# Kernel optimization log

Measured on AMD Instinct MI355X. Metric: run time of the kernel, lower is better.

## Reference

```python
import jax, jax.numpy as jnp
import numpy as np

L, H, D, HS, DFF, V, B, T = 4, 16, 1024, 64, 5120, 32000, 2, 1024
EPS = 1e-5


def setup_inputs() -> dict:
    key = jax.random.key(0)
    ks = iter(jax.random.split(key, 40))
    def nrm(shape):
        return jax.random.normal(next(ks), shape, dtype=jnp.float32) * 0.02
    inp = {}
    inp['idx'] = jax.random.randint(next(ks), (B, T), 0, V)
    inp['tok_emb'] = nrm((V, D))
    inp['pos_emb'] = nrm((T, D))
    for s in ('u', 'm'):  # u = unmasked heads, m = masked (causal) heads
        inp['Wq_' + s] = nrm((L, H, D, HS)); inp['bq_' + s] = jnp.zeros((L, H, HS), jnp.float32)
        inp['Wk_' + s] = nrm((L, H, D, HS)); inp['bk_' + s] = jnp.zeros((L, H, HS), jnp.float32)
        inp['Wv_' + s] = nrm((L, H, D, HS)); inp['bv_' + s] = jnp.zeros((L, H, HS), jnp.float32)
        inp['Wp_' + s] = nrm((L, D, D));     inp['bp_' + s] = jnp.zeros((L, D), jnp.float32)
    inp['W1'] = nrm((L, D, DFF)); inp['b1'] = jnp.zeros((L, DFF), jnp.float32)
    inp['W2'] = nrm((L, DFF, D)); inp['b2'] = jnp.zeros((L, D), jnp.float32)
    ones = jnp.ones((L, D), jnp.float32); zer = jnp.zeros((L, D), jnp.float32)
    inp['lnf_g'] = ones; inp['lnf_b'] = zer     # LayerNorm inside FeedForward
    inp['n1_g'] = ones;  inp['n1_b'] = zer      # Block.norm1
    inp['n2_g'] = ones;  inp['n2_b'] = zer      # Block.norm2
    inp['nf_g'] = jnp.ones((D,), jnp.float32); inp['nf_b'] = jnp.zeros((D,), jnp.float32)
    inp['Wfin'] = nrm((D, V)); inp['bfin'] = jnp.zeros((V,), jnp.float32)
    return inp


def _ln(x, g, b):
    mu = jnp.mean(x, -1, keepdims=True)
    var = jnp.mean((x - mu) ** 2, -1, keepdims=True)
    return (x - mu) / jnp.sqrt(var + EPS) * g + b


def _attn(xn, Wq, bq, Wk, bk, Wv, bv, Wp, bp, causal):
    # xn: [B,T,D]; Wq/Wk/Wv: [H,D,HS] (all heads batched in one einsum)
    q = jnp.einsum('btd,hde->bhte', xn, Wq) + bq[:, None, :]
    k = jnp.einsum('btd,hde->bhte', xn, Wk) + bk[:, None, :]
    v = jnp.einsum('btd,hde->bhte', xn, Wv) + bv[:, None, :]
    w = jnp.einsum('bhte,bhse->bhts', q, k) * (HS ** -0.5)
    if causal:
        mask = jnp.tril(jnp.ones((w.shape[-2], w.shape[-1]), bool))
        w = jnp.where(mask, w, -jnp.inf)
    w = jax.nn.softmax(w, axis=-1)
    o = jnp.einsum('bhts,bhse->bhte', w, v)
    o = o.transpose(0, 2, 1, 3).reshape(xn.shape[0], xn.shape[1], -1)  # concat heads
    return o @ Wp + bp


def _ffn(x, W1, b1, W2, b2, g, b):
    h = jax.nn.leaky_relu(x @ W1 + b1, negative_slope=0.01)
    return _ln(h @ W2 + b2, g, b)


def reference(idx, tok_emb, pos_emb,
              Wq_u, bq_u, Wk_u, bk_u, Wv_u, bv_u, Wp_u, bp_u,
              Wq_m, bq_m, Wk_m, bk_m, Wv_m, bv_m, Wp_m, bp_m,
              W1, b1, W2, b2, lnf_g, lnf_b, n1_g, n1_b, n2_g, n2_b,
              nf_g, nf_b, Wfin, bfin):
    Tn = idx.shape[1]
    x = tok_emb[idx] + pos_emb[:Tn]
    for l in range(L):
        # exact quirky Block wiring from the original code
        x2 = x + _attn(_ln(x, n1_g[l], n1_b[l]), Wq_u[l], bq_u[l], Wk_u[l], bk_u[l],
                       Wv_u[l], bv_u[l], Wp_u[l], bp_u[l], False)
        x = x2 + _ln(_ffn(_ln(x2, n2_g[l], n2_b[l]), W1[l], b1[l], W2[l], b2[l],
                          lnf_g[l], lnf_b[l]), n1_g[l], n1_b[l])
        x2 = x + _attn(_ln(x, n1_g[l], n1_b[l]), Wq_m[l], bq_m[l], Wk_m[l], bk_m[l],
                       Wv_m[l], bv_m[l], Wp_m[l], bp_m[l], True)
        x = x2 + _ln(_ffn(_ln(x2, n2_g[l], n2_b[l]), W1[l], b1[l], W2[l], b2[l],
                          lnf_g[l], lnf_b[l]), n2_g[l], n2_b[l])
    x = _ln(x, nf_g, nf_b)
    return x @ Wfin + bfin  # logits [B,T,V]; targets=None path -> loss is None
```

## Files before the change

kernel.cpp:

```cpp
#include <hip/hip_runtime.h>
#include <hip/hip_bf16.h>
#include <math.h>

#define LNUM 4
#define H 16
#define D 1024
#define HS 64
#define DFF 5120
#define V 32000
#define BB 2
#define T 1024
#define M (BB*T)
#define EPS 1e-5f

typedef __attribute__((ext_vector_type(8))) short bf16x8;
typedef __attribute__((ext_vector_type(4))) float f32x4;

__device__ __forceinline__ void gload16(const void* g, void* l) {
    __builtin_amdgcn_global_load_lds(
        (const __attribute__((address_space(1))) void*)g,
        (__attribute__((address_space(3))) void*)l, 16, 0, 0);
}

__device__ __forceinline__ float wred_sum(float v) {
    #pragma unroll
    for (int off = 32; off; off >>= 1) v += __shfl_xor(v, off, 64);
    return v;
}

__global__ __launch_bounds__(256) void embed_kernel(const int* __restrict__ idx,
        const float* __restrict__ tok, const float* __restrict__ pos,
        float* __restrict__ x) {
    int row = blockIdx.x;
    int t = row & (T - 1);
    int tok_id = idx[row];
    int c = threadIdx.x * 4;
    float4 a = *(const float4*)&tok[(size_t)tok_id * D + c];
    float4 p = *(const float4*)&pos[(size_t)t * D + c];
    a.x += p.x; a.y += p.y; a.z += p.z; a.w += p.w;
    *(float4*)&x[(size_t)row * D + c] = a;
}

__global__ __launch_bounds__(256) void ln_bf16_w4_kernel(const float* __restrict__ in,
        const float* __restrict__ g, const float* __restrict__ b,
        __hip_bfloat16* __restrict__ out) {
    int w = threadIdx.x >> 6, lane = threadIdx.x & 63;
    int row = blockIdx.x * 4 + w;
    const float* rp = in + (size_t)row * D;
    float4 xv[4];
    float s = 0.f;
    #pragma unroll
    for (int c = 0; c < 4; ++c) {
        xv[c] = *(const float4*)&rp[c * 256 + lane * 4];
        s += xv[c].x + xv[c].y + xv[c].z + xv[c].w;
    }
    float mu = wred_sum(s) * (1.0f / D);
    float vs = 0.f;
    #pragma unroll
    for (int c = 0; c < 4; ++c) {
        xv[c].x -= mu; xv[c].y -= mu; xv[c].z -= mu; xv[c].w -= mu;
        vs += xv[c].x*xv[c].x + xv[c].y*xv[c].y + xv[c].z*xv[c].z + xv[c].w*xv[c].w;
    }
    float rs = rsqrtf(wred_sum(vs) * (1.0f / D) + EPS);
    #pragma unroll
    for (int c = 0; c < 4; ++c) {
        int j = c * 256 + lane * 4;
        float4 gv = *(const float4*)&g[j];
        float4 bv = *(const float4*)&b[j];
        union { ushort4 u4; __hip_bfloat16 h[4]; } pk;
        pk.h[0] = __float2bfloat16(xv[c].x * rs * gv.x + bv.x);
        pk.h[1] = __float2bfloat16(xv[c].y * rs * gv.y + bv.y);
        pk.h[2] = __float2bfloat16(xv[c].z * rs * gv.z + bv.z);
        pk.h[3] = __float2bfloat16(xv[c].w * rs * gv.w + bv.w);
        *(ushort4*)&out[(size_t)row * D + j] = pk.u4;
    }
}

template<int NP>
__global__ __launch_bounds__(256) void ffn_tail_kernel(
        const float* __restrict__ part, const float* __restrict__ b2,
        const float* __restrict__ g1, const float* __restrict__ b1,
        const float* __restrict__ g2, const float* __restrict__ b2g,
        const float* __restrict__ res, float* __restrict__ xout,
        const float* __restrict__ gn, const float* __restrict__ bn,
        __hip_bfloat16* __restrict__ xnout) {
    const size_t MD = (size_t)M * D;
    int w = threadIdx.x >> 6, lane = threadIdx.x & 63;
    int row = blockIdx.x * 4 + w;
    size_t ro = (size_t)row * D;
    float4 f[4];
    float s = 0.f;
    #pragma unroll
    for (int c = 0; c < 4; ++c) {
        int j = c * 256 + lane * 4;
        float4 acc = *(const float4*)&b2[j];
        #pragma unroll
        for (int pI = 0; pI < NP; ++pI) {
            float4 pv = *(const float4*)&part[pI * MD + ro + j];
            acc.x += pv.x; acc.y += pv.y; acc.z += pv.z; acc.w += pv.w;
        }
        f[c] = acc;
        s += acc.x + acc.y + acc.z + acc.w;
    }
    float mu = wred_sum(s) * (1.0f / D);
    float vs = 0.f;
    #pragma unroll
    for (int c = 0; c < 4; ++c) {
        f[c].x -= mu; f[c].y -= mu; f[c].z -= mu; f[c].w -= mu;
        vs += f[c].x*f[c].x + f[c].y*f[c].y + f[c].z*f[c].z + f[c].w*f[c].w;
    }
    float rs = rsqrtf(wred_sum(vs) * (1.0f / D) + EPS);
    float s2 = 0.f;
    #pragma unroll
    for (int c = 0; c < 4; ++c) {
        int j = c * 256 + lane * 4;
        float4 gv = *(const float4*)&g1[j];
        float4 bv = *(const float4*)&b1[j];
        f[c].x = f[c].x * rs * gv.x + bv.x;
        f[c].y = f[c].y * rs * gv.y + bv.y;
        f[c].z = f[c].z * rs * gv.z + bv.z;
        f[c].w = f[c].w * rs * gv.w + bv.w;
        s2 += f[c].x + f[c].y + f[c].z + f[c].w;
    }
    float mu2 = wred_sum(s2) * (1.0f / D);
    float vs2 = 0.f;
    #pragma unroll
    for (int c = 0; c < 4; ++c) {
        f[c].x -= mu2; f[c].y -= mu2; f[c].z -= mu2; f[c].w -= mu2;
        vs2 += f[c].x*f[c].x + f[c].y*f[c].y + f[c].z*f[c].z + f[c].w*f[c].w;
    }
    float rs2 = rsqrtf(wred_sum(vs2) * (1.0f / D) + EPS);
    float s3 = 0.f;
    #pragma unroll
    for (int c = 0; c < 4; ++c) {
        int j = c * 256 + lane * 4;
        float4 gv = *(const float4*)&g2[j];
        float4 bv = *(const float4*)&b2g[j];
        float4 rv = *(const float4*)&res[ro + j];
        f[c].x = rv.x + f[c].x * rs2 * gv.x + bv.x;
        f[c].y = rv.y + f[c].y * rs2 * gv.y + bv.y;
        f[c].z = rv.z + f[c].z * rs2 * gv.z + bv.z;
        f[c].w = rv.w + f[c].w * rs2 * gv.w + bv.w;
        *(float4*)&xout[ro + j] = f[c];
        s3 += f[c].x + f[c].y + f[c].z + f[c].w;
    }
    float mu3 = wred_sum(s3) * (1.0f / D);
    float vs3 = 0.f;
    #pragma unroll
    for (int c = 0; c < 4; ++c) {
        f[c].x -= mu3; f[c].y -= mu3; f[c].z -= mu3; f[c].w -= mu3;
        vs3 += f[c].x*f[c].x + f[c].y*f[c].y + f[c].z*f[c].z + f[c].w*f[c].w;
    }
    float rs3 = rsqrtf(wred_sum(vs3) * (1.0f / D) + EPS);
    #pragma unroll
    for (int c = 0; c < 4; ++c) {
        int j = c * 256 + lane * 4;
        float4 gv = *(const float4*)&gn[j];
        float4 bv = *(const float4*)&bn[j];
        union { ushort4 u4; __hip_bfloat16 h[4]; } pk;
        pk.h[0] = __float2bfloat16(f[c].x * rs3 * gv.x + bv.x);
        pk.h[1] = __float2bfloat16(f[c].y * rs3 * gv.y + bv.y);
        pk.h[2] = __float2bfloat16(f[c].z * rs3 * gv.z + bv.z);
        pk.h[3] = __float2bfloat16(f[c].w * rs3 * gv.w + bv.w);
        *(ushort4*)&xnout[ro + j] = pk.u4;
    }
}

__global__ __launch_bounds__(256) void transpose_bf16_kernel(
        const float* __restrict__ in, __hip_bfloat16* __restrict__ out,
        int R, int C, size_t zin, size_t zout) {
    __shared__ float t[32][33];
    in += (size_t)blockIdx.z * zin; out += (size_t)blockIdx.z * zout;
    int tx = threadIdx.x & 31, ty = threadIdx.x >> 5;
    int c0 = blockIdx.x * 32, r0 = blockIdx.y * 32;
    #pragma unroll
    for (int i = 0; i < 4; ++i)
        t[ty + i * 8][tx] = in[(size_t)(r0 + ty + i * 8) * C + c0 + tx];
    __syncthreads();
    #pragma unroll
    for (int i = 0; i < 4; ++i)
        out[(size_t)(c0 + ty + i * 8) * R + r0 + tx] = __float2bfloat16(t[tx][ty + i * 8]);
}

__global__ __launch_bounds__(256) void transpose_qkv_kernel(
        const float* __restrict__ Wq, const float* __restrict__ Wk,
        const float* __restrict__ Wv, short* __restrict__ outT) {
    __shared__ float t[32][33];
    int z = blockIdx.z;
    int which = z >> 4, h = z & 15;
    const float* in = (which == 0 ? Wq : which == 1 ? Wk : Wv) + (size_t)h * D * HS;
    __hip_bfloat16* out = (__hip_bfloat16*)outT + ((size_t)which * H + h) * HS * D;
    int tx = threadIdx.x & 31, ty = threadIdx.x >> 5;
    int c0 = blockIdx.x * 32, r0 = blockIdx.y * 32;
    #pragma unroll
    for (int i = 0; i < 4; ++i)
        t[ty + i * 8][tx] = in[(size_t)(r0 + ty + i * 8) * HS + c0 + tx];
    __syncthreads();
    #pragma unroll
    for (int i = 0; i < 4; ++i)
        out[(size_t)(c0 + ty + i * 8) * D + r0 + tx] = __float2bfloat16(t[tx][ty + i * 8]);
}

__global__ __launch_bounds__(256) void transpose_v_kernel(const short* __restrict__ in,
        short* __restrict__ out) {
    __shared__ short t[32][33];
    int z = blockIdx.z;
    in  += (size_t)z * T * HS;
    out += (size_t)z * HS * T;
    int tx = threadIdx.x & 31, ty = threadIdx.x >> 5;
    int c0 = blockIdx.x * 32, r0 = blockIdx.y * 32;
    #pragma unroll
    for (int i = 0; i < 4; ++i)
        t[ty + i * 8][tx] = in[(size_t)(r0 + ty + i * 8) * HS + c0 + tx];
    __syncthreads();
    #pragma unroll
    for (int i = 0; i < 4; ++i)
        out[(size_t)(c0 + ty + i * 8) * T + r0 + tx] = t[tx][ty + i * 8];
}

template<int BM, int EPI>
__global__ __launch_bounds__(256) void mm_bf16_kernel(
        const short* __restrict__ A, const short* __restrict__ BT,
        const float* __restrict__ bias0, const float* __restrict__ bias1,
        const float* __restrict__ bias2, const float* __restrict__ res,
        float* __restrict__ C0, float* __restrict__ C1, float* __restrict__ C2,
        __hip_bfloat16* __restrict__ Cbf, int N, int Kloop, int lda) {
    constexpr int BK = 64, BN = 128;
    constexpr int MI = BM / 32;
    __shared__ __align__(16) char As[2][BM * 128];
    __shared__ __align__(16) char Bs[2][BN * 128];
    int nwg = gridDim.x * gridDim.y;
    int bid = blockIdx.y * gridDim.x + blockIdx.x;
    int bx = blockIdx.x, by = blockIdx.y;
    if (!(nwg & 7)) {
        int s = (bid & 7) * (nwg >> 3) + (bid >> 3);
        bx = s % gridDim.x; by = s / gridDim.x;
    }
    int tid = threadIdx.x;
    int lane = tid & 63, wid = tid >> 6;
    int wr = wid >> 1, wc = wid & 1;
    int l15 = lane & 15, l16 = lane >> 4;
    int m0 = bx * BM, n0 = by * BN;
    f32x4 acc[MI][4] = {};

    const size_t lda2 = (size_t)lda * 2;
    const char* Agc = (const char*)A + (size_t)m0 * lda2 + (size_t)blockIdx.z * Kloop * 2;
    const char* Bgc = (const char*)BT + (size_t)n0 * lda2 + (size_t)blockIdx.z * Kloop * 2;

    auto stage = [&](int buf, int kbyte) {
        #pragma unroll
        for (int i = 0; i < BM / 32; ++i) {
            int o = i * 4096 + tid * 16;
            int row = o >> 7, col = o & 127;
            gload16(Agc + (size_t)row * lda2 + kbyte + (col ^ ((row & 7) << 4)),
                    As[buf] + o);
        }
        #pragma unroll
        for (int i = 0; i < 4; ++i) {
            int o = i * 4096 + tid * 16;
            int row = o >> 7, col = o & 127;
            gload16(Bgc + (size_t)row * lda2 + kbyte + (col ^ ((row & 7) << 4)),
                    Bs[buf] + o);
        }
    };
    auto compute = [&](int buf) {
        #pragma unroll
        for (int kk = 0; kk < 2; ++kk) {
            bf16x8 af[MI], bfr[4];
            #pragma unroll
            for (int mi = 0; mi < MI; ++mi) {
                int row = wr * (BM / 2) + mi * 16 + l15;
                af[mi] = *(const bf16x8*)(As[buf] + row * 128 +
                          ((kk * 64 + l16 * 16) ^ ((row & 7) << 4)));
            }
            #pragma unroll
            for (int ni = 0; ni < 4; ++ni) {
                int row = wc * 64 + ni * 16 + l15;
                bfr[ni] = *(const bf16x8*)(Bs[buf] + row * 128 +
                          ((kk * 64 + l16 * 16) ^ ((row & 7) << 4)));
            }
            __builtin_amdgcn_s_setprio(1);
            #pragma unroll
            for (int mi = 0; mi < MI; ++mi)
                #pragma unroll
                for (int ni = 0; ni < 4; ++ni)
                    acc[mi][ni] = __builtin_amdgcn_mfma_f32_16x16x32_bf16(
                        af[mi], bfr[ni], acc[mi][ni], 0, 0, 0);
            __builtin_amdgcn_s_setprio(0);
        }
    };

    const int NT = Kloop / BK;
    stage(0, 0);
    stage(1, 128);
    for (int t = 0; t < NT; ++t) {
        if (t < NT - 1) {
            if constexpr (BM == 128) asm volatile("s_waitcnt vmcnt(8)" ::: "memory");
            else                     asm volatile("s_waitcnt vmcnt(6)" ::: "memory");
        } else {
            asm volatile("s_waitcnt vmcnt(0)" ::: "memory");
        }
        __builtin_amdgcn_sched_barrier(0);
        __builtin_amdgcn_s_barrier();
        __builtin_amdgcn_sched_barrier(0);
        compute(t & 1);
        __builtin_amdgcn_s_barrier();
        __builtin_amdgcn_sched_barrier(0);
        if (t + 2 < NT) stage(t & 1, (t + 2) * 128);
    }

    int rbase = m0 + wr * (BM / 2) + l16 * 4;
    int cbase = n0 + wc * 64 + l15;
    size_t zoff = (EPI == 4) ? (size_t)blockIdx.z * M * N : 0;
    #pragma unroll
    for (int mi = 0; mi < MI; ++mi) {
        #pragma unroll
        for (int ni = 0; ni < 4; ++ni) {
            int col = cbase + ni * 16;
            float bv = 0.f;
            if (EPI == 3) {
                int z = col >> 10, nn = col & 1023;
                bv = (z == 0 ? bias0 : z == 1 ? bias1 : bias2)[nn];
            } else if (EPI != 4) bv = bias0[col];
            #pragma unroll
            for (int r = 0; r < 4; ++r) {
                int row = rbase + mi * 16 + r;
                float v = acc[mi][ni][r] + bv;
                if (EPI == 0) {
                    C0[(size_t)row * N + col] = v;
                } else if (EPI == 1) {
                    C0[(size_t)row * N + col] = v + res[(size_t)row * N + col];
                } else if (EPI == 2) {
                    v = v > 0.f ? v : 0.01f * v;
                    Cbf[(size_t)row * N + col] = __float2bfloat16(v);
                } else if (EPI == 4) {
                    C0[zoff + (size_t)row * N + col] = v;
                } else {
                    int z = col >> 10;
                    int hh = (col >> 6) & 15, e = col & 63;
                    int b = row >> 10, t = row & (T - 1);
                    __hip_bfloat16* dst = (__hip_bfloat16*)(z == 0 ? C0 : (z == 1 ? C1 : C2));
                    dst[(((size_t)(b * H + hh)) * T + t) * HS + e] = __float2bfloat16(v);
                }
            }
        }
    }
}

template<int CAUSAL>
__global__ __launch_bounds__(256) void attn_mfma_kernel(
        const short* __restrict__ q, const short* __restrict__ k,
        const short* __restrict__ vt, __hip_bfloat16* __restrict__ att) {
    __shared__ __align__(16) short Ks[128 * 64];
    __shared__ __align__(16) short Vs[64 * 128];
    __shared__ __align__(16) short Ps[4][16 * 128];
    int bh = blockIdx.y;
    int bI = bh >> 4, h = bh & 15;
    int tix = blockIdx.x;
    if (CAUSAL) tix = (tix & 1) ? (15 - (tix >> 1)) : (tix >> 1);
    int t0 = tix * 64;
    int tid = threadIdx.x;
    int lane = tid & 63, w = tid >> 6;
    int l15 = lane & 15, l16 = lane >> 4;

    const short* Qg = q + ((size_t)bh * T + t0 + w * 16 + l15) * HS + l16 * 8;
    bf16x8 qf0 = *(const bf16x8*)Qg;
    bf16x8 qf1 = *(const bf16x8*)(Qg + 32);

    const char* Kg = (const char*)(k + (size_t)bh * T * HS);
    const char* Vg = (const char*)(vt + (size_t)bh * HS * T);

    float m_run[4] = {-1e30f, -1e30f, -1e30f, -1e30f};
    float l_run[4] = {0.f, 0.f, 0.f, 0.f};
    f32x4 acc_o[4] = {};
    char* Pw = (char*)Ps[w];
    int pswz = l15 << 4;

    int n_tiles = CAUSAL ? (t0 / 128 + 1) : (T / 128);
    for (int it = 0; it < n_tiles; ++it) {
        int s0 = it * 128;
        __syncthreads();
        #pragma unroll
        for (int i = 0; i < 4; ++i) {
            int o = i * 4096 + tid * 16;
            int row = o >> 7, bir = o & 127;
            gload16(Kg + (size_t)(s0 + row) * 128 + (bir ^ ((row & 7) << 4)),
                    (char*)Ks + o);
        }
        #pragma unroll
        for (int i = 0; i < 4; ++i) {
            int o = i * 4096 + tid * 16;
            int row = o >> 8, bb = o & 255;
            gload16(Vg + (size_t)row * 2048 + s0 * 2 + (bb ^ ((row & 15) << 4)),
                    (char*)Vs + o);
        }
        __syncthreads();

        f32x4 acc_s[8] = {};
        __builtin_amdgcn_s_setprio(1);
        #pragma unroll
        for (int c = 0; c < 8; ++c) {
            int row = c * 16 + l15;
            const char* kb_ = (const char*)Ks + row * 128;
            int swz = (row & 7) << 4;
            bf16x8 kf0 = *(const bf16x8*)(kb_ + ((l16 * 16) ^ swz));
            bf16x8 kf1 = *(const bf16x8*)(kb_ + ((64 + l16 * 16) ^ swz));
            acc_s[c] = __builtin_amdgcn_mfma_f32_16x16x32_bf16(qf0, kf0, acc_s[c], 0, 0, 0);
            acc_s[c] = __builtin_amdgcn_mfma_f32_16x16x32_bf16(qf1, kf1, acc_s[c], 0, 0, 0);
        }
        __builtin_amdgcn_s_setprio(0);

        bool domask = CAUSAL && (it == n_tiles - 1);
        #pragma unroll
        for (int r = 0; r < 4; ++r) {
            float sc[8];
            #pragma unroll
            for (int c = 0; c < 8; ++c) {
                float s = acc_s[c][r];
                if (domask && (s0 + c * 16 + l15) > (t0 + w * 16 + l16 * 4 + r)) s = -1e30f;
                sc[c] = s;
            }
            float tm = fmaxf(fmaxf(fmaxf(sc[0], sc[1]), fmaxf(sc[2], sc[3])),
                             fmaxf(fmaxf(sc[4], sc[5]), fmaxf(sc[6], sc[7])));
            tm = fmaxf(tm, __shfl_xor(tm, 1, 16));
            tm = fmaxf(tm, __shfl_xor(tm, 2, 16));
            tm = fmaxf(tm, __shfl_xor(tm, 4, 16));
            tm = fmaxf(tm, __shfl_xor(tm, 8, 16));
            float mn = fmaxf(m_run[r], tm);
            int prow = l16 * 4 + r;
            int pswzr = prow << 4;
            float ls = 0.f;
            #pragma unroll
            for (int c = 0; c < 8; ++c) {
                float pv = __expf(0.125f * (sc[c] - mn));
                int pbyte = prow * 256 + (((c * 16 + l15) * 2) ^ pswzr);
                *(__hip_bfloat16*)(Pw + pbyte) = __float2bfloat16(pv);
                ls += pv;
            }
            ls += __shfl_xor(ls, 1, 16);
            ls += __shfl_xor(ls, 2, 16);
            ls += __shfl_xor(ls, 4, 16);
            ls += __shfl_xor(ls, 8, 16);
            float alpha = __expf(0.125f * (m_run[r] - mn));
            l_run[r] = l_run[r] * alpha + ls;
            m_run[r] = mn;
            acc_o[0][r] *= alpha; acc_o[1][r] *= alpha;
            acc_o[2][r] *= alpha; acc_o[3][r] *= alpha;
        }

        const char* Pb = Pw + l15 * 256;
        bf16x8 pa[4];
        #pragma unroll
        for (int t = 0; t < 4; ++t)
            pa[t] = *(const bf16x8*)(Pb + ((t * 64 + l16 * 16) ^ pswz));
        __builtin_amdgcn_s_setprio(1);
        #pragma unroll
        for (int ni = 0; ni < 4; ++ni) {
            int row = ni * 16 + l15;
            const char* vb_ = (const char*)Vs + row * 256;
            int swz = (row & 15) << 4;
            #pragma unroll
            for (int t = 0; t < 4; ++t) {
                bf16x8 vf = *(const bf16x8*)(vb_ + ((t * 64 + l16 * 16) ^ swz));
                acc_o[ni] = __builtin_amdgcn_mfma_f32_16x16x32_bf16(pa[t], vf, acc_o[ni], 0, 0, 0);
            }
        }
        __builtin_amdgcn_s_setprio(0);
    }

    float inv[4];
    #pragma unroll
    for (int r = 0; r < 4; ++r) inv[r] = 1.0f / l_run[r];
    #pragma unroll
    for (int ni = 0; ni < 4; ++ni) {
        #pragma unroll
        for (int r = 0; r < 4; ++r) {
            size_t orow = ((size_t)(bI * T) + t0 + w * 16 + l16 * 4 + r) * D
                        + h * HS + ni * 16 + l15;
            att[orow] = __float2bfloat16(acc_o[ni][r] * inv[r]);
        }
    }
}

extern "C" void kernel_launch(void* const* d_in, const int* in_sizes, int n_in,
                              void* d_out, int out_size, void* d_ws, size_t ws_size,
                              hipStream_t stream) {
    const int*   idx     = (const int*)d_in[0];
    const float* tok_emb = (const float*)d_in[1];
    const float* pos_emb = (const float*)d_in[2];
    const float* Wq_u = (const float*)d_in[3],  *bq_u = (const float*)d_in[4];
    const float* Wk_u = (const float*)d_in[5],  *bk_u = (const float*)d_in[6];
    const float* Wv_u = (const float*)d_in[7],  *bv_u = (const float*)d_in[8];
    const float* Wp_u = (const float*)d_in[9],  *bp_u = (const float*)d_in[10];
    const float* Wq_m = (const float*)d_in[11], *bq_m = (const float*)d_in[12];
    const float* Wk_m = (const float*)d_in[13], *bk_m = (const float*)d_in[14];
    const float* Wv_m = (const float*)d_in[15], *bv_m = (const float*)d_in[16];
    const float* Wp_m = (const float*)d_in[17], *bp_m = (const float*)d_in[18];
    const float* W1   = (const float*)d_in[19], *b1   = (const float*)d_in[20];
    const float* W2   = (const float*)d_in[21], *b2   = (const float*)d_in[22];
    const float* lnf_g = (const float*)d_in[23], *lnf_b = (const float*)d_in[24];
    const float* n1_g  = (const float*)d_in[25], *n1_b  = (const float*)d_in[26];
    const float* n2_g  = (const float*)d_in[27], *n2_b  = (const float*)d_in[28];
    const float* nf_g  = (const float*)d_in[29], *nf_b  = (const float*)d_in[30];
    const float* Wfin  = (const float*)d_in[31], *bfin  = (const float*)d_in[32];
    float* out = (float*)d_out;

    char* p = (char*)d_ws;
    auto alloc = [&](size_t bytes) { char* r = p; p += (bytes + 255) & ~255ull; return r; };
    float* x    = (float*)alloc((size_t)M * D * 4);
    float* x2   = (float*)alloc((size_t)M * D * 4);
    float* w2p  = (float*)alloc((size_t)4 * M * D * 4);
    short* qbf  = (short*)alloc((size_t)M * D * 2);
    short* kbf  = (short*)alloc((size_t)M * D * 2);
    short* vbf  = (short*)alloc((size_t)M * D * 2);
    short* vtb  = (short*)alloc((size_t)M * D * 2);
    short* xnb  = (short*)alloc((size_t)M * D * 2);
    short* attb = (short*)alloc((size_t)M * D * 2);
    short* hb   = (short*)alloc((size_t)M * DFF * 2);
    short* WqkvT= (short*)alloc((size_t)3 * 1024 * 1024 * 2);
    short* WpT  = (short*)alloc((size_t)1024 * 1024 * 2);
    short* W1T  = (short*)alloc((size_t)D * DFF * 2);
    short* W2T  = (short*)alloc((size_t)DFF * D * 2);
    short* WfT  = (short*)alloc((size_t)D * V * 2);

    embed_kernel<<<M, 256, 0, stream>>>(idx, tok_emb, pos_emb, x);
    ln_bf16_w4_kernel<<<M / 4, 256, 0, stream>>>(x, n1_g, n1_b, (__hip_bfloat16*)xnb);
    transpose_bf16_kernel<<<dim3(V / 32, D / 32, 1), 256, 0, stream>>>(
        Wfin, (__hip_bfloat16*)WfT, D, V, 0, 0);

    for (int l = 0; l < LNUM; ++l) {
        const float *n1g = n1_g + l * D, *n1b = n1_b + l * D;
        const float *n2g = n2_g + l * D, *n2b = n2_b + l * D;
        const float *lfg = lnf_g + l * D, *lfb = lnf_b + l * D;
        const float *W1l = W1 + (size_t)l * D * DFF, *b1l = b1 + l * DFF;
        const float *W2l = W2 + (size_t)l * DFF * D, *b2l = b2 + l * D;
        transpose_bf16_kernel<<<dim3(DFF / 32, D / 32, 1), 256, 0, stream>>>(
            W1l, (__hip_bfloat16*)W1T, D, DFF, 0, 0);
        transpose_bf16_kernel<<<dim3(D / 32, DFF / 32, 1), 256, 0, stream>>>(
            W2l, (__hip_bfloat16*)W2T, DFF, D, 0, 0);
        for (int half = 0; half < 2; ++half) {
            const float *Wq_, *bq_, *Wk_, *bk_, *Wv_, *bv_, *Wp_, *bp_;
            if (half == 0) { Wq_ = Wq_u; bq_ = bq_u; Wk_ = Wk_u; bk_ = bk_u;
                             Wv_ = Wv_u; bv_ = bv_u; Wp_ = Wp_u; bp_ = bp_u; }
            else           { Wq_ = Wq_m; bq_ = bq_m; Wk_ = Wk_m; bk_ = bk_m;
                             Wv_ = Wv_m; bv_ = bv_m; Wp_ = Wp_m; bp_ = bp_m; }
            Wq_ += (size_t)l * H * D * HS;  bq_ += l * H * HS;
            Wk_ += (size_t)l * H * D * HS;  bk_ += l * H * HS;
            Wv_ += (size_t)l * H * D * HS;  bv_ += l * H * HS;
            Wp_ += (size_t)l * D * D;       bp_ += l * D;

            transpose_qkv_kernel<<<dim3(HS / 32, D / 32, 48), 256, 0, stream>>>(
                Wq_, Wk_, Wv_, WqkvT);
            transpose_bf16_kernel<<<dim3(D / 32, D / 32, 1), 256, 0, stream>>>(
                Wp_, (__hip_bfloat16*)WpT, D, D, 0, 0);

            mm_bf16_kernel<128, 3><<<dim3(M / 128, 3072 / 128), 256, 0, stream>>>(
                xnb, WqkvT, bq_, bk_, bv_, nullptr,
                (float*)qbf, (float*)kbf, (float*)vbf, nullptr, 3072, D, D);
            transpose_v_kernel<<<dim3(HS / 32, T / 32, BB * H), 256, 0, stream>>>(vbf, vtb);
            if (half == 0)
                attn_mfma_kernel<0><<<dim3(T / 64, BB * H), 256, 0, stream>>>(
                    qbf, kbf, vtb, (__hip_bfloat16*)attb);
            else
                attn_mfma_kernel<1><<<dim3(T / 64, BB * H), 256, 0, stream>>>(
                    qbf, kbf, vtb, (__hip_bfloat16*)attb);
            mm_bf16_kernel<64, 1><<<dim3(M / 64, D / 128), 256, 0, stream>>>(
                attb, WpT, bp_, nullptr, nullptr, x, x2, nullptr, nullptr, nullptr, D, D, D);
            ln_bf16_w4_kernel<<<M / 4, 256, 0, stream>>>(x2, n2g, n2b, (__hip_bfloat16*)xnb);
            mm_bf16_kernel<128, 2><<<dim3(M / 128, DFF / 128), 256, 0, stream>>>(
                xnb, W1T, b1l, nullptr, nullptr, nullptr, nullptr, nullptr, nullptr,
                (__hip_bfloat16*)hb, DFF, D, D);
            mm_bf16_kernel<128, 4><<<dim3(M / 128, D / 128, 4), 256, 0, stream>>>(
                hb, W2T, nullptr, nullptr, nullptr, nullptr, w2p, nullptr, nullptr,
                nullptr, D, DFF / 4, DFF);
            const float* og = half ? n2g : n1g;
            const float* ob = half ? n2b : n1b;
            const float* gn; const float* bn;
            if (half == 0)      { gn = n1g; bn = n1b; }
            else if (l < LNUM-1){ gn = n1_g + (l+1)*D; bn = n1_b + (l+1)*D; }
            else                { gn = nf_g; bn = nf_b; }
            ffn_tail_kernel<4><<<M / 4, 256, 0, stream>>>(
                w2p, b2l, lfg, lfb, og, ob, x2, x, gn, bn, (__hip_bfloat16*)xnb);
        }
    }
    mm_bf16_kernel<128, 0><<<dim3(M / 128, V / 128), 256, 0, stream>>>(
        xnb, WfT, bfin, nullptr, nullptr, nullptr, out, nullptr, nullptr, nullptr, V, D, D);
}
```

Measured before the change: 1.650 ms.

## Add 256x256-tile 512-thread GEMM kernel for FFN up-projection and logits

Adds a new GEMM kernel with 256x256 output tiles, 8 waves per block, K split into two 32-wide halves with interleaved LDS staging and MFMA phases, and XCD-aware block remapping. It replaces the 128x128 kernel for the W1 up-projection (with leaky-ReLU bf16 epilogue) and the final vocabulary projection. Larger tiles raise arithmetic intensity and cut redundant global/L2 traffic for these large GEMMs. The cost is heavier register pressure, fewer blocks (160 for W1, 1000 for logits), and a mapping that hardcodes M/256 = 8 row tiles.

```diff
diff --git a/kernel.cpp b/kernel.cpp
--- a/kernel.cpp
+++ b/kernel.cpp
@@ -218,6 +218,138 @@
         out[(size_t)(c0 + ty + i * 8) * T + r0 + tx] = t[tx][ty + i * 8];
 }
 
+template<int EPI>
+__global__ __launch_bounds__(512, 2) void mm256_kernel(
+        const short* __restrict__ A, const short* __restrict__ BT,
+        const float* __restrict__ bias0, float* __restrict__ C0,
+        __hip_bfloat16* __restrict__ Cbf, int N, int Kloop, int lda) {
+    __shared__ __align__(16) char LA[2][2][256 * 64];
+    __shared__ __align__(16) char LB[2][2][256 * 64];
+    int tid = threadIdx.x;
+    int lane = tid & 63, wid = tid >> 6;
+    int wr = wid >> 2, wc = wid & 3;
+    int l15 = lane & 15, l16 = lane >> 4;
+
+    int nwg = gridDim.x;
+    int bid = blockIdx.x;
+    int q = nwg >> 3, r = nwg & 7;
+    int xcd = bid & 7, loc = bid >> 3;
+    int wg = (xcd < r ? xcd * (q + 1) : r * (q + 1) + (xcd - r) * q) + loc;
+    int m0 = (wg & 7) * 256;
+    int n0 = (wg >> 3) * 256;
+
+    const size_t lda2 = (size_t)lda * 2;
+    const char* Agc = (const char*)A + (size_t)m0 * lda2;
+    const char* Bgc = (const char*)BT + (size_t)n0 * lda2;
+
+    f32x4 acc[8][4] = {};
+    bf16x8 af[8], bfr[2];
+
+    auto stA = [&](int buf, int kh, int kt) {
+        #pragma unroll
+        for (int i = 0; i < 2; ++i) {
+            int o = i * 8192 + tid * 16;
+            int row = o >> 6, col = o & 63;
+            gload16(Agc + (size_t)row * lda2 + kt * 128 + kh * 64 +
+                    (col ^ (((row >> 1) & 3) << 4)), LA[buf][kh] + o);
+        }
+    };
+    auto stB = [&](int buf, int kh, int kt) {
+        #pragma unroll
+        for (int i = 0; i < 2; ++i) {
+            int o = i * 8192 + tid * 16;
+            int row = o >> 6, col = o & 63;
+            gload16(Bgc + (size_t)row * lda2 + kt * 128 + kh * 64 +
+                    (col ^ (((row >> 1) & 3) << 4)), LB[buf][kh] + o);
+        }
+    };
+    auto rdA = [&](int buf, int kk) {
+        #pragma unroll
+        for (int mf = 0; mf < 8; ++mf) {
+            int row = wr * 128 + mf * 16 + l15;
+            af[mf] = *(const bf16x8*)(LA[buf][kk] + row * 64 +
+                      ((l16 * 16) ^ (((row >> 1) & 3) << 4)));
+        }
+    };
+    auto rdB = [&](int buf, int kk, int nh) {
+        #pragma unroll
+        for (int nf = 0; nf < 2; ++nf) {
+            int row = wc * 64 + nh * 32 + nf * 16 + l15;
+            bfr[nf] = *(const bf16x8*)(LB[buf][kk] + row * 64 +
+                       ((l16 * 16) ^ (((row >> 1) & 3) << 4)));
+        }
+    };
+    auto mfma16 = [&](int nh) {
+        __builtin_amdgcn_s_setprio(1);
+        #pragma unroll
+        for (int mf = 0; mf < 8; ++mf) {
+            acc[mf][nh * 2 + 0] = __builtin_amdgcn_mfma_f32_16x16x32_bf16(
+                af[mf], bfr[0], acc[mf][nh * 2 + 0], 0, 0, 0);
+            acc[mf][nh * 2 + 1] = __builtin_amdgcn_mfma_f32_16x16x32_bf16(
+                af[mf], bfr[1], acc[mf][nh * 2 + 1], 0, 0, 0);
+        }
+        __builtin_amdgcn_s_setprio(0);
+        __builtin_amdgcn_s_barrier();
+    };
+
+    const int NT = Kloop / 64;
+    stA(0, 0, 0); stB(0, 0, 0); stA(0, 1, 0); stB(0, 1, 0);
+    stA(1, 0, 1); stB(1, 0, 1);
+
+    for (int t = 0; t < NT; ++t) {
+        int buf = t & 1;
+        if (t + 1 < NT) { asm volatile("s_waitcnt vmcnt(4)" ::: "memory"); }
+        else            { asm volatile("s_waitcnt vmcnt(0)" ::: "memory"); }
+        __builtin_amdgcn_sched_barrier(0);
+        __builtin_amdgcn_s_barrier();
+        __builtin_amdgcn_sched_barrier(0);
+        rdA(buf, 0); rdB(buf, 0, 0);
+        if (t + 1 < NT) stA(buf ^ 1, 1, t + 1);
+        __builtin_amdgcn_s_barrier();
+        asm volatile("s_waitcnt lgkmcnt(0)" ::: "memory");
+        __builtin_amdgcn_sched_barrier(0);
+        mfma16(0);
+        rdB(buf, 0, 1);
+        if (t + 1 < NT) stB(buf ^ 1, 1, t + 1);
+        __builtin_amdgcn_s_barrier();
+        asm volatile("s_waitcnt lgkmcnt(0)" ::: "memory");
+        __builtin_amdgcn_sched_barrier(0);
+        mfma16(1);
+        rdA(buf, 1); rdB(buf, 1, 0);
+        if (t + 2 < NT) stA(buf, 0, t + 2);
+        __builtin_amdgcn_s_barrier();
+        asm volatile("s_waitcnt lgkmcnt(0)" ::: "memory");
+        __builtin_amdgcn_sched_barrier(0);
+        mfma16(0);
+        rdB(buf, 1, 1);
+        if (t + 2 < NT) stB(buf, 0, t + 2);
+        __builtin_amdgcn_s_barrier();
+        asm volatile("s_waitcnt lgkmcnt(0)" ::: "memory");
+        __builtin_amdgcn_sched_barrier(0);
+        mfma16(1);
+    }
+
+    #pragma unroll
+    for (int mf = 0; mf < 8; ++mf) {
+        #pragma unroll
+        for (int nf = 0; nf < 4; ++nf) {
+            int col = n0 + wc * 64 + nf * 16 + l15;
+            float bv = bias0[col];
+            #pragma unroll
+            for (int rr = 0; rr < 4; ++rr) {
+                int row = m0 + wr * 128 + mf * 16 + l16 * 4 + rr;
+                float v = acc[mf][nf][rr] + bv;
+                if (EPI == 0) {
+                    C0[(size_t)row * N + col] = v;
+                } else {
+                    v = v > 0.f ? v : 0.01f * v;
+                    Cbf[(size_t)row * N + col] = __float2bfloat16(v);
+                }
+            }
+        }
+    }
+}
+
 template<int BM, int EPI>
 __global__ __launch_bounds__(256) void mm_bf16_kernel(
         const short* __restrict__ A, const short* __restrict__ BT,
@@ -225,10 +357,9 @@
         const float* __restrict__ bias2, const float* __restrict__ res,
         float* __restrict__ C0, float* __restrict__ C1, float* __restrict__ C2,
         __hip_bfloat16* __restrict__ Cbf, int N, int Kloop, int lda) {
-    constexpr int BK = 64, BN = 128;
     constexpr int MI = BM / 32;
     __shared__ __align__(16) char As[2][BM * 128];
-    __shared__ __align__(16) char Bs[2][BN * 128];
+    __shared__ __align__(16) char Bs[2][128 * 128];
     int nwg = gridDim.x * gridDim.y;
     int bid = blockIdx.y * gridDim.x + blockIdx.x;
     int bx = blockIdx.x, by = blockIdx.y;
@@ -240,7 +371,7 @@
     int lane = tid & 63, wid = tid >> 6;
     int wr = wid >> 1, wc = wid & 1;
     int l15 = lane & 15, l16 = lane >> 4;
-    int m0 = bx * BM, n0 = by * BN;
+    int m0 = bx * BM, n0 = by * 128;
     f32x4 acc[MI][4] = {};
 
     const size_t lda2 = (size_t)lda * 2;
@@ -290,7 +421,7 @@
         }
     };
 
-    const int NT = Kloop / BK;
+    const int NT = Kloop / 64;
     stage(0, 0);
     stage(1, 128);
     for (int t = 0; t < NT; ++t) {
@@ -338,9 +469,9 @@
                 } else {
                     int z = col >> 10;
                     int hh = (col >> 6) & 15, e = col & 63;
-                    int b = row >> 10, t = row & (T - 1);
+                    int b = row >> 10, t2 = row & (T - 1);
                     __hip_bfloat16* dst = (__hip_bfloat16*)(z == 0 ? C0 : (z == 1 ? C1 : C2));
-                    dst[(((size_t)(b * H + hh)) * T + t) * HS + e] = __float2bfloat16(v);
+                    dst[(((size_t)(b * H + hh)) * T + t2) * HS + e] = __float2bfloat16(v);
                 }
             }
         }
@@ -567,9 +698,8 @@
             mm_bf16_kernel<64, 1><<<dim3(M / 64, D / 128), 256, 0, stream>>>(
                 attb, WpT, bp_, nullptr, nullptr, x, x2, nullptr, nullptr, nullptr, D, D, D);
             ln_bf16_w4_kernel<<<M / 4, 256, 0, stream>>>(x2, n2g, n2b, (__hip_bfloat16*)xnb);
-            mm_bf16_kernel<128, 2><<<dim3(M / 128, DFF / 128), 256, 0, stream>>>(
-                xnb, W1T, b1l, nullptr, nullptr, nullptr, nullptr, nullptr, nullptr,
-                (__hip_bfloat16*)hb, DFF, D, D);
+            mm256_kernel<2><<<(M / 256) * (DFF / 256), 512, 0, stream>>>(
+                xnb, W1T, b1l, nullptr, (__hip_bfloat16*)hb, DFF, D, D);
             mm_bf16_kernel<128, 4><<<dim3(M / 128, D / 128, 4), 256, 0, stream>>>(
                 hb, W2T, nullptr, nullptr, nullptr, nullptr, w2p, nullptr, nullptr,
                 nullptr, D, DFF / 4, DFF);
@@ -583,6 +713,6 @@
                 w2p, b2l, lfg, lfb, og, ob, x2, x, gn, bn, (__hip_bfloat16*)xnb);
         }
     }
-    mm_bf16_kernel<128, 0><<<dim3(M / 128, V / 128), 256, 0, stream>>>(
-        xnb, WfT, bfin, nullptr, nullptr, nullptr, out, nullptr, nullptr, nullptr, V, D, D);
-}
+    mm256_kernel<0><<<(M / 256) * (V / 256), 512, 0, stream>>>(
+        xnb, WfT, bfin, out, nullptr, V, D, D);
+}
```

Result: faster. 1.589 ms (-3.7%).
